# Kernel optimization log

Measured on AMD Instinct MI355X. Metric: run time of the kernel, lower is better.

## Reference

```python
import jax, jax.numpy as jnp
import numpy as np

N_NODES = 100000
N_EDGES = 3200000
N_GRAPHS = 64
IN_FEATS = 128
DIM = 32
N_LAYERS = 4


def setup_inputs() -> dict:
    key = jax.random.key(0)
    ks = jax.random.split(key, 16)
    x = jax.random.normal(ks[0], (N_NODES, IN_FEATS), dtype=jnp.float32)
    src = jax.random.randint(ks[1], (N_EDGES,), 0, N_NODES)
    dst = jax.random.randint(ks[2], (N_EDGES,), 0, N_NODES)
    graph_ids = jnp.sort(jax.random.randint(ks[3], (N_NODES,), 0, N_GRAPHS))
    s = 1.0 / np.sqrt(IN_FEATS)
    s2 = 1.0 / np.sqrt(DIM)
    Wn0 = jax.random.uniform(ks[4], (IN_FEATS, DIM), jnp.float32, -s, s)
    bn0 = jnp.zeros((DIM,), jnp.float32)
    Ws0 = jax.random.uniform(ks[5], (IN_FEATS, DIM), jnp.float32, -s, s)
    Wn = jax.random.uniform(ks[6], (N_LAYERS - 1, DIM, DIM), jnp.float32, -s2, s2)
    bn = jnp.zeros((N_LAYERS - 1, DIM), jnp.float32)
    Ws = jax.random.uniform(ks[7], (N_LAYERS - 1, DIM, DIM), jnp.float32, -s2, s2)
    Wfc1 = jax.random.uniform(ks[8], (DIM, 8), jnp.float32, -s2, s2)
    bfc1 = jnp.zeros((8,), jnp.float32)
    Wout = jax.random.uniform(ks[9], (8, 4), jnp.float32, -1/np.sqrt(8), 1/np.sqrt(8))
    bout = jnp.zeros((4,), jnp.float32)
    return {"x": x, "Wn0": Wn0, "bn0": bn0, "Ws0": Ws0,
            "Wn": Wn, "bn": bn, "Ws": Ws,
            "Wfc1": Wfc1, "bfc1": bfc1, "Wout": Wout, "bout": bout,
            "src": src, "dst": dst, "graph_ids": graph_ids}


def _conv_layer(h, Wn_, bn_, Ws_, src, dst):
    # GraphConv(norm='none'): transform then sum over incoming edges (src -> dst)
    rhs = h @ Wn_                                   # [N, out]
    neigh = jax.ops.segment_sum(rhs[src], dst, num_segments=N_NODES) + bn_
    self_feat = h @ Ws_                             # Linear, no bias
    return jax.nn.relu(neigh + self_feat)


def reference(x, Wn0, bn0, Ws0, Wn, bn, Ws, Wfc1, bfc1, Wout, bout, src, dst, graph_ids):
    h = _conv_layer(x, Wn0, bn0, Ws0, src, dst)
    for i in range(N_LAYERS - 1):
        h = _conv_layer(h, Wn[i], bn[i], Ws[i], src, dst)
    # per-graph sum pooling (dgl.sum_nodes over batched graph)
    hg = jax.ops.segment_sum(h, graph_ids, num_segments=N_GRAPHS)  # [G, 32]
    hg2 = jax.nn.relu(hg @ Wfc1 + bfc1)
    out = jax.nn.relu(hg2 @ Wout + bout)
    return jax.nn.softmax(out, axis=1)
```

## Files before the change

kernel.cpp:

```cpp
#include <hip/hip_runtime.h>
#include <hip/hip_bf16.h>
#include <math.h>


#define TILE_NODES 256
#define CE 12800
#define SCAN_CHUNK 2048
#define MAX_NB 1024
#define SENT 131071

__device__ inline unsigned char f2fp8(float f) {
    unsigned u = __float_as_uint(f);
    unsigned s = (u >> 24) & 0x80u;
    float a = fminf(fabsf(f), 448.f);
    unsigned v = __float_as_uint(a * 0x1p-120f);
    v = v + 0xFFFFFu + ((v >> 20) & 1u);
    return (unsigned char)(s | ((v >> 20) & 0x7Fu));
}
__device__ inline float fp8_dec(unsigned x) {
    unsigned v = ((x & 0x80u) << 24) | ((x & 0x7Fu) << 20);
    return __uint_as_float(v) * 0x1p120f;
}

typedef float v2f __attribute__((ext_vector_type(2)));
typedef _Float16 h2 __attribute__((ext_vector_type(2)));
typedef __fp16 p2 __attribute__((ext_vector_type(2)));
union U32H2 { unsigned u; h2 h; p2 p; };

__device__ inline unsigned packh2(float a, float b) {
#if __has_builtin(__builtin_amdgcn_cvt_pkrtz)
    U32H2 t; t.p = __builtin_amdgcn_cvt_pkrtz(a, b); return t.u;
#else
    U32H2 t; t.h.x = (_Float16)a; t.h.y = (_Float16)b; return t.u;
#endif
}
__device__ inline float dot2(unsigned a, unsigned b, float c) {
    U32H2 ua, ub; ua.u = a; ub.u = b;
#if __has_builtin(__builtin_amdgcn_fdot2)
    return __builtin_amdgcn_fdot2(ua.h, ub.h, c, false);
#else
    return c + (float)ua.h.x * (float)ub.h.x + (float)ua.h.y * (float)ub.h.y;
#endif
}

__device__ inline void acc8_fp8(unsigned w0, unsigned w1, float4& a0, float4& a1) {
#if __has_builtin(__builtin_amdgcn_cvt_pk_f32_fp8)
    v2f p0 = __builtin_amdgcn_cvt_pk_f32_fp8(w0, 0);
    v2f p1 = __builtin_amdgcn_cvt_pk_f32_fp8(w0, 1);
    v2f p2v = __builtin_amdgcn_cvt_pk_f32_fp8(w1, 0);
    v2f p3 = __builtin_amdgcn_cvt_pk_f32_fp8(w1, 1);
    a0.x += p0.x; a0.y += p0.y; a0.z += p1.x; a0.w += p1.y;
    a1.x += p2v.x; a1.y += p2v.y; a1.z += p3.x; a1.w += p3.y;
#else
    a0.x += fp8_dec(w0 & 0xFFu);         a0.y += fp8_dec((w0 >> 8) & 0xFFu);
    a0.z += fp8_dec((w0 >> 16) & 0xFFu); a0.w += fp8_dec(w0 >> 24);
    a1.x += fp8_dec(w1 & 0xFFu);         a1.y += fp8_dec((w1 >> 8) & 0xFFu);
    a1.z += fp8_dec((w1 >> 16) & 0xFFu); a1.w += fp8_dec(w1 >> 24);
#endif
}

__global__ __launch_bounds__(1024) void k_hist2(
    const int* __restrict__ dst, int* __restrict__ histT,
    int n_edges, int NB, int C)
{
    __shared__ int hist[MAX_NB];
    const int c = blockIdx.x;
    for (int b = threadIdx.x; b < NB; b += 1024) hist[b] = 0;
    __syncthreads();
    const int beg = c * CE;
    const int end = min(beg + CE, n_edges);
    for (int e = beg + threadIdx.x; e < end; e += 1024)
        atomicAdd(&hist[dst[e] >> 8], 1);
    __syncthreads();
    for (int b = threadIdx.x; b < NB; b += 1024)
        histT[b * C + c] = hist[b];
}

__global__ __launch_bounds__(256) void k_chunk_sum(
    const int* __restrict__ v, int* __restrict__ part, int n)
{
    __shared__ int red[256];
    const int base = blockIdx.x * SCAN_CHUNK;
    int s = 0;
    for (int i = threadIdx.x; i < SCAN_CHUNK; i += 256) {
        int idx = base + i;
        if (idx < n) s += v[idx];
    }
    red[threadIdx.x] = s;
    __syncthreads();
    for (int off = 128; off > 0; off >>= 1) {
        if (threadIdx.x < off) red[threadIdx.x] += red[threadIdx.x + off];
        __syncthreads();
    }
    if (threadIdx.x == 0) part[blockIdx.x] = red[0];
}

__global__ void k_scan_part(int* __restrict__ part, int nparts)
{
    if (threadIdx.x == 0 && blockIdx.x == 0) {
        int run = 0;
        for (int i = 0; i < nparts; ++i) { int v = part[i]; part[i] = run; run += v; }
    }
}

__global__ __launch_bounds__(256) void k_write_off(
    const int* __restrict__ v, const int* __restrict__ part,
    int* __restrict__ off, int n, int total)
{
    __shared__ int lds[256];
    const int tid   = threadIdx.x;
    const int base  = blockIdx.x * SCAN_CHUNK;
    const int tbase = base + tid * 8;
    int c[8];
    int tot = 0;
#pragma unroll
    for (int m = 0; m < 8; ++m) {
        int idx = tbase + m;
        c[m] = (idx < n) ? v[idx] : 0;
        tot += c[m];
    }
    lds[tid] = tot;
    __syncthreads();
    for (int o = 1; o < 256; o <<= 1) {
        int val = (tid >= o) ? lds[tid - o] : 0;
        __syncthreads();
        lds[tid] += val;
        __syncthreads();
    }
    int run = part[blockIdx.x] + lds[tid] - tot;
#pragma unroll
    for (int m = 0; m < 8; ++m) {
        int idx = tbase + m;
        if (idx < n) off[idx] = run;
        run += c[m];
    }
    if (blockIdx.x == 0 && tid == 0) off[n] = total;
}

__global__ __launch_bounds__(1024) void k_binfill(
    const int* __restrict__ src, const int* __restrict__ dst,
    const int* __restrict__ off, unsigned int* __restrict__ ebuf,
    int n_edges, int NB, int C)
{
    __shared__ int lcur[MAX_NB];
    const int c = blockIdx.x;
    for (int b = threadIdx.x; b < NB; b += 1024)
        lcur[b] = off[b * C + c];
    __syncthreads();
    const int beg = c * CE;
    const int end = min(beg + CE, n_edges);
    for (int e = beg + threadIdx.x; e < end; e += 1024) {
        const int d = dst[e];
        const int b = d >> 8;
        const unsigned int dl = (unsigned int)(d & 255);
        const int pos = atomicAdd(&lcur[b], 1);
        ebuf[pos] = (dl << 17) | (unsigned int)src[e];
    }
}

__global__ __launch_bounds__(1024) void k_tile_sort(
    const int* __restrict__ off, const unsigned int* __restrict__ ebuf,
    int* __restrict__ eidx, int* __restrict__ ptrb, int* __restrict__ ptre,
    int n_nodes, int NB, int C, int n_edges)
{
    __shared__ int hist[TILE_NODES];
    __shared__ int phist[TILE_NODES];
    __shared__ int scan[TILE_NODES];
    __shared__ int cur[TILE_NODES];
    const int t = blockIdx.x;
    const int beg = off[t * C];
    const int end = (t + 1 < NB) ? off[(t + 1) * C] : n_edges;
    const int tb  = ((beg + 3) & ~3) + 1024 * t;
    const int node_base = t * TILE_NODES;
    const int n_valid = min(TILE_NODES, n_nodes - node_base);

    if (threadIdx.x < TILE_NODES) hist[threadIdx.x] = 0;
    __syncthreads();
    for (int e = beg + threadIdx.x; e < end; e += 1024)
        atomicAdd(&hist[ebuf[e] >> 17], 1);
    __syncthreads();
    if (threadIdx.x < TILE_NODES) {
        const int ph = (hist[threadIdx.x] + 3) & ~3;
        phist[threadIdx.x] = ph;
        scan[threadIdx.x]  = ph;
    }
    __syncthreads();
    for (int o = 1; o < TILE_NODES; o <<= 1) {
        int v = 0;
        if (threadIdx.x < TILE_NODES && threadIdx.x >= o) v = scan[threadIdx.x - o];
        __syncthreads();
        if (threadIdx.x < TILE_NODES) scan[threadIdx.x] += v;
        __syncthreads();
    }
    if (threadIdx.x < TILE_NODES) {
        const int ex = scan[threadIdx.x] - phist[threadIdx.x];
        cur[threadIdx.x] = ex;
        if (threadIdx.x < n_valid) {
            ptrb[node_base + threadIdx.x] = tb + ex;
            ptre[node_base + threadIdx.x] = tb + ex + phist[threadIdx.x];
        }
    }
    __syncthreads();
    for (int e = beg + threadIdx.x; e < end; e += 1024) {
        const unsigned int v = ebuf[e];
        const int dl = (int)(v >> 17);
        const int pos = tb + atomicAdd(&cur[dl], 1);
        eidx[pos] = (int)(v & 0x1FFFFu);
    }
    __syncthreads();
    if (threadIdx.x < n_valid) {
        int p  = tb + cur[threadIdx.x];
        const int pe = tb + scan[threadIdx.x];
        for (; p < pe; ++p) eidx[p] = SENT;
    }
}

__global__ __launch_bounds__(256, 4) void k_layer0(
    const float* __restrict__ x, const float* __restrict__ Wn0,
    const float* __restrict__ bn0, const float* __restrict__ Ws0,
    unsigned char* __restrict__ Ab, float* __restrict__ B, int n_nodes)
{
    __shared__ unsigned sWn[64 * 32];
    __shared__ unsigned sWs[64 * 32];
    __shared__ unsigned sx[32 * 64];

    for (int i = threadIdx.x; i < 64 * 32; i += 256) {
        const int k2 = i >> 5, jj = i & 31;
        sWn[i] = packh2(Wn0[(2 * k2) * 32 + jj], Wn0[(2 * k2 + 1) * 32 + jj]);
        sWs[i] = packh2(Ws0[(2 * k2) * 32 + jj], Ws0[(2 * k2 + 1) * 32 + jj]);
    }
    const int tile = blockIdx.x * 32;
    {
        const float4* s4 = (const float4*)(x + (size_t)tile * 128);
        const int lim = (n_nodes - tile) * 32;
#pragma unroll
        for (int m = 0; m < 4; ++m) {
            int i = threadIdx.x + m * 256;
            if (i < lim) {
                float4 v = s4[i];
                const int row = i >> 5, q = i & 31;
                sx[row * 64 + 2 * q]     = packh2(v.x, v.y);
                sx[row * 64 + 2 * q + 1] = packh2(v.z, v.w);
            }
        }
    }
    const int j = threadIdx.x & 31;
    const int r = threadIdx.x >> 5;
    const float bias = bn0[j];
    __syncthreads();

    float accA[4] = {0.f, 0.f, 0.f, 0.f};
    float accB[4] = {bias, bias, bias, bias};
#pragma unroll 2
    for (int k2 = 0; k2 < 64; k2 += 4) {
        const unsigned wn0 = sWn[(k2 + 0) * 32 + j], ws0 = sWs[(k2 + 0) * 32 + j];
        const unsigned wn1 = sWn[(k2 + 1) * 32 + j], ws1 = sWs[(k2 + 1) * 32 + j];
        const unsigned wn2 = sWn[(k2 + 2) * 32 + j], ws2 = sWs[(k2 + 2) * 32 + j];
        const unsigned wn3 = sWn[(k2 + 3) * 32 + j], ws3 = sWs[(k2 + 3) * 32 + j];
#pragma unroll
        for (int m = 0; m < 4; ++m) {
            const uint4 xv = *(const uint4*)(sx + (r + 8 * m) * 64 + k2);
            accA[m] = dot2(xv.x, wn0, accA[m]);
            accA[m] = dot2(xv.y, wn1, accA[m]);
            accA[m] = dot2(xv.z, wn2, accA[m]);
            accA[m] = dot2(xv.w, wn3, accA[m]);
            accB[m] = dot2(xv.x, ws0, accB[m]);
            accB[m] = dot2(xv.y, ws1, accB[m]);
            accB[m] = dot2(xv.z, ws2, accB[m]);
            accB[m] = dot2(xv.w, ws3, accB[m]);
        }
    }
#pragma unroll
    for (int m = 0; m < 4; ++m) {
        const int node = tile + r + 8 * m;
        if (node < n_nodes) {
            Ab[(size_t)node * 32 + j] = f2fp8(accA[m]);
            B[(size_t)node * 32 + j] = accB[m];
        }
    }
}

__global__ __launch_bounds__(256, 4) void k_layer(
    float* HB,
    const float* __restrict__ Wn, const float* __restrict__ bnv,
    const float* __restrict__ Ws, unsigned char* __restrict__ Ab, int n_nodes)
{
    __shared__ unsigned sWn[16 * 32];
    __shared__ unsigned sWs[16 * 32];
    __shared__ unsigned sh[64 * 16];

    for (int i = threadIdx.x; i < 16 * 32; i += 256) {
        const int k2 = i >> 5, jj = i & 31;
        sWn[i] = packh2(Wn[(2 * k2) * 32 + jj], Wn[(2 * k2 + 1) * 32 + jj]);
        sWs[i] = packh2(Ws[(2 * k2) * 32 + jj], Ws[(2 * k2 + 1) * 32 + jj]);
    }
    const int tile = blockIdx.x * 64;
    {
        const float4* s4 = (const float4*)(HB + (size_t)tile * 32);
        const int lim = (n_nodes - tile) * 8;
#pragma unroll
        for (int m = 0; m < 2; ++m) {
            int i = threadIdx.x + m * 256;
            if (i < lim) {
                float4 v = s4[i];
                v.x = fmaxf(v.x, 0.f); v.y = fmaxf(v.y, 0.f);
                v.z = fmaxf(v.z, 0.f); v.w = fmaxf(v.w, 0.f);
                const int row = i >> 3, q = i & 7;
                sh[row * 16 + 2 * q]     = packh2(v.x, v.y);
                sh[row * 16 + 2 * q + 1] = packh2(v.z, v.w);
            }
        }
    }
    const int j = threadIdx.x & 31;
    const int r = threadIdx.x >> 5;
    const float bias = bnv[j];
    __syncthreads();

    float accA[8] = {0.f};
    float accB[8];
#pragma unroll
    for (int m = 0; m < 8; ++m) accB[m] = bias;
#pragma unroll 2
    for (int k2 = 0; k2 < 16; k2 += 4) {
        const unsigned wn0 = sWn[(k2 + 0) * 32 + j], ws0 = sWs[(k2 + 0) * 32 + j];
        const unsigned wn1 = sWn[(k2 + 1) * 32 + j], ws1 = sWs[(k2 + 1) * 32 + j];
        const unsigned wn2 = sWn[(k2 + 2) * 32 + j], ws2 = sWs[(k2 + 2) * 32 + j];
        const unsigned wn3 = sWn[(k2 + 3) * 32 + j], ws3 = sWs[(k2 + 3) * 32 + j];
#pragma unroll
        for (int m = 0; m < 8; ++m) {
            const uint4 hv = *(const uint4*)(sh + (r + 8 * m) * 16 + k2);
            accA[m] = dot2(hv.x, wn0, accA[m]);
            accA[m] = dot2(hv.y, wn1, accA[m]);
            accA[m] = dot2(hv.z, wn2, accA[m]);
            accA[m] = dot2(hv.w, wn3, accA[m]);
            accB[m] = dot2(hv.x, ws0, accB[m]);
            accB[m] = dot2(hv.y, ws1, accB[m]);
            accB[m] = dot2(hv.z, ws2, accB[m]);
            accB[m] = dot2(hv.w, ws3, accB[m]);
        }
    }
#pragma unroll
    for (int m = 0; m < 8; ++m) {
        const int node = tile + r + 8 * m;
        if (node < n_nodes) {
            Ab[(size_t)node * 32 + j] = f2fp8(accA[m]);
            HB[(size_t)node * 32 + j] = accB[m];
        }
    }
}

__global__ __launch_bounds__(256) void k_agg3(
    const int* __restrict__ ptrb, const int* __restrict__ ptre,
    const int* __restrict__ eidx,
    const unsigned char* __restrict__ Ab, float* __restrict__ B, int n_nodes)
{
    const int g    = blockIdx.x * 64 + (threadIdx.x >> 2);
    const int lane = threadIdx.x & 3;
    if (g >= n_nodes) return;
    const int beg = ptrb[g];
    const int end = ptre[g];
    const uint2* __restrict__ A2 = (const uint2*)Ab;
    const int4* __restrict__ E4 = (const int4*)eidx;
    float4* B4 = (float4*)B;

    float4 a0 = B4[(size_t)g * 8 + lane * 2 + 0];
    float4 a1 = B4[(size_t)g * 8 + lane * 2 + 1];
    int e4 = beg >> 2;
    const int n4 = end >> 2;
    for (; e4 + 4 <= n4; e4 += 4) {
        const int4 q0 = E4[e4 + 0];
        const int4 q1 = E4[e4 + 1];
        const int4 q2 = E4[e4 + 2];
        const int4 q3 = E4[e4 + 3];
        uint2 rw;
        rw = A2[(size_t)q0.x * 4 + lane]; acc8_fp8(rw.x, rw.y, a0, a1);
        rw = A2[(size_t)q0.y * 4 + lane]; acc8_fp8(rw.x, rw.y, a0, a1);
        rw = A2[(size_t)q0.z * 4 + lane]; acc8_fp8(rw.x, rw.y, a0, a1);
        rw = A2[(size_t)q0.w * 4 + lane]; acc8_fp8(rw.x, rw.y, a0, a1);
        rw = A2[(size_t)q1.x * 4 + lane]; acc8_fp8(rw.x, rw.y, a0, a1);
        rw = A2[(size_t)q1.y * 4 + lane]; acc8_fp8(rw.x, rw.y, a0, a1);
        rw = A2[(size_t)q1.z * 4 + lane]; acc8_fp8(rw.x, rw.y, a0, a1);
        rw = A2[(size_t)q1.w * 4 + lane]; acc8_fp8(rw.x, rw.y, a0, a1);
        rw = A2[(size_t)q2.x * 4 + lane]; acc8_fp8(rw.x, rw.y, a0, a1);
        rw = A2[(size_t)q2.y * 4 + lane]; acc8_fp8(rw.x, rw.y, a0, a1);
        rw = A2[(size_t)q2.z * 4 + lane]; acc8_fp8(rw.x, rw.y, a0, a1);
        rw = A2[(size_t)q2.w * 4 + lane]; acc8_fp8(rw.x, rw.y, a0, a1);
        rw = A2[(size_t)q3.x * 4 + lane]; acc8_fp8(rw.x, rw.y, a0, a1);
        rw = A2[(size_t)q3.y * 4 + lane]; acc8_fp8(rw.x, rw.y, a0, a1);
        rw = A2[(size_t)q3.z * 4 + lane]; acc8_fp8(rw.x, rw.y, a0, a1);
        rw = A2[(size_t)q3.w * 4 + lane]; acc8_fp8(rw.x, rw.y, a0, a1);
    }
    for (; e4 < n4; ++e4) {
        const int4 q = E4[e4];
        uint2 rw;
        rw = A2[(size_t)q.x * 4 + lane]; acc8_fp8(rw.x, rw.y, a0, a1);
        rw = A2[(size_t)q.y * 4 + lane]; acc8_fp8(rw.x, rw.y, a0, a1);
        rw = A2[(size_t)q.z * 4 + lane]; acc8_fp8(rw.x, rw.y, a0, a1);
        rw = A2[(size_t)q.w * 4 + lane]; acc8_fp8(rw.x, rw.y, a0, a1);
    }
    B4[(size_t)g * 8 + lane * 2 + 0] = a0;
    B4[(size_t)g * 8 + lane * 2 + 1] = a1;
}

__global__ __launch_bounds__(256) void k_zero_f(float* __restrict__ p, int n)
{
    int i = blockIdx.x * 256 + threadIdx.x;
    if (i < n) p[i] = 0.f;
}

__global__ __launch_bounds__(256) void k_pool1(
    const float* __restrict__ H, const int* __restrict__ gids,
    float* __restrict__ hg, int n_nodes)
{
    const int base = blockIdx.x * 128;
    const int lim  = min(base + 128, n_nodes);
    const int j = threadIdx.x & 31;
    const int r = threadIdx.x >> 5;

    int curg = -1;
    float acc = 0.f;
    for (int n = base + r; n < lim; n += 8) {
        const int g = gids[n];
        const float v = fmaxf(H[(size_t)n * 32 + j], 0.f);
        if (g != curg) {
            if (curg >= 0) atomicAdd(&hg[curg * 32 + j], acc);
            curg = g;
            acc = v;
        } else {
            acc += v;
        }
    }
    if (curg >= 0) atomicAdd(&hg[curg * 32 + j], acc);
}

__global__ __launch_bounds__(64) void k_head(
    const float* __restrict__ hg,
    const float* __restrict__ Wfc1, const float* __restrict__ bfc1,
    const float* __restrict__ Wout, const float* __restrict__ bout,
    float* __restrict__ out, int n_graphs)
{
    const int g = blockIdx.x * blockDim.x + threadIdx.x;
    if (g >= n_graphs) return;
    float h[32];
#pragma unroll
    for (int k = 0; k < 32; ++k) h[k] = hg[g * 32 + k];
    float z[8];
#pragma unroll
    for (int m = 0; m < 8; ++m) {
        float a = bfc1[m];
#pragma unroll
        for (int k = 0; k < 32; ++k) a += h[k] * Wfc1[k * 8 + m];
        z[m] = fmaxf(a, 0.f);
    }
    float o[4];
#pragma unroll
    for (int q = 0; q < 4; ++q) {
        float a = bout[q];
#pragma unroll
        for (int m = 0; m < 8; ++m) a += z[m] * Wout[m * 4 + q];
        o[q] = fmaxf(a, 0.f);
    }
    const float mx = fmaxf(fmaxf(o[0], o[1]), fmaxf(o[2], o[3]));
    const float e0 = expf(o[0] - mx), e1 = expf(o[1] - mx);
    const float e2 = expf(o[2] - mx), e3 = expf(o[3] - mx);
    const float inv = 1.f / (e0 + e1 + e2 + e3);
    out[g * 4 + 0] = e0 * inv;
    out[g * 4 + 1] = e1 * inv;
    out[g * 4 + 2] = e2 * inv;
    out[g * 4 + 3] = e3 * inv;
}

extern "C" void kernel_launch(void* const* d_in, const int* in_sizes, int n_in,
                              void* d_out, int out_size, void* d_ws, size_t ws_size,
                              hipStream_t stream)
{
    const float* x    = (const float*)d_in[0];
    const float* Wn0  = (const float*)d_in[1];
    const float* bn0  = (const float*)d_in[2];
    const float* Ws0  = (const float*)d_in[3];
    const float* Wn   = (const float*)d_in[4];
    const float* bn   = (const float*)d_in[5];
    const float* Ws   = (const float*)d_in[6];
    const float* Wfc1 = (const float*)d_in[7];
    const float* bfc1 = (const float*)d_in[8];
    const float* Wout = (const float*)d_in[9];
    const float* bout = (const float*)d_in[10];
    const int*   src  = (const int*)d_in[11];
    const int*   dst  = (const int*)d_in[12];
    const int*   gids = (const int*)d_in[13];

    const int n_nodes  = in_sizes[0] / 128;
    const int n_edges  = in_sizes[11];
    const int n_graphs = out_size / 4;
    const size_t N32 = (size_t)n_nodes * 32;
    const size_t AB_ROWS = 131072;

    const int NB = (n_nodes + TILE_NODES - 1) / TILE_NODES;
    const int C  = (n_edges + CE - 1) / CE;
    const int n_off = NB * C;

    unsigned char* Ab = (unsigned char*)d_ws;
    float* B   = (float*)(Ab + AB_ROWS * 32);
    float* hg  = B + N32;
    int* histT = (int*)(hg + (size_t)n_graphs * 32);
    int* off   = histT + n_off;
    int* part  = off + n_off + 1;
    int* ptrb  = part + 256;
    int* ptre  = ptrb + n_nodes;
    unsigned int* ebuf = (unsigned int*)(ptre + n_nodes);
    int* eidx  = (int*)(ebuf + n_edges);

    const int nparts = (n_off + SCAN_CHUNK - 1) / SCAN_CHUNK;

    k_hist2<<<C, 1024, 0, stream>>>(dst, histT, n_edges, NB, C);
    k_chunk_sum<<<nparts, 256, 0, stream>>>(histT, part, n_off);
    k_scan_part<<<1, 64, 0, stream>>>(part, nparts);
    k_write_off<<<nparts, 256, 0, stream>>>(histT, part, off, n_off, n_edges);
    k_binfill<<<C, 1024, 0, stream>>>(src, dst, off, ebuf, n_edges, NB, C);
    k_tile_sort<<<NB, 1024, 0, stream>>>(off, ebuf, eidx, ptrb, ptre,
                                         n_nodes, NB, C, n_edges);
    k_zero_f<<<1, 256, 0, stream>>>((float*)(Ab + (size_t)SENT * 32), 8);

    const int mblocks0 = (n_nodes + 31) / 32;
    const int mblocks  = (n_nodes + 63) / 64;
    const int ablocks  = (n_nodes + 63) / 64;

    k_layer0<<<mblocks0, 256, 0, stream>>>(x, Wn0, bn0, Ws0, Ab, B, n_nodes);
    k_agg3<<<ablocks, 256, 0, stream>>>(ptrb, ptre, eidx, Ab, B, n_nodes);

    for (int l = 0; l < 3; ++l) {
        k_layer<<<mblocks, 256, 0, stream>>>(B, Wn + l * 1024, bn + l * 32,
                                             Ws + l * 1024, Ab, n_nodes);
        k_agg3<<<ablocks, 256, 0, stream>>>(ptrb, ptre, eidx, Ab, B, n_nodes);
    }

    k_zero_f<<<(n_graphs * 32 + 255) / 256, 256, 0, stream>>>(hg, n_graphs * 32);
    k_pool1<<<(n_nodes + 127) / 128, 256, 0, stream>>>(B, gids, hg, n_nodes);
    k_head<<<(n_graphs + 63) / 64, 64, 0, stream>>>(hg, Wfc1, bfc1, Wout, bout,
                                                    (float*)d_out, n_graphs);
}
```

Before: 367.6 us.

## Use MFMA f16 matrix cores for per-layer node transforms with prepacked weights

Replaces the dot2-based scalar matmuls in the layer kernels with 16x16x32 f16 MFMA instructions, with each wave handling 16 nodes. A new small kernel prepacks the weights once into MFMA B-fragment layout in fp16, so blocks no longer rebuild shared-memory weight tables. Layer 0 now processes 64 nodes per block and uses an XOR-swizzled shared tile to limit bank conflicts. The workspace is also realigned to 256-byte boundaries. The dense transforms are a small share of the total next to the edge aggregation and sorting, so the overall effect is bounded.

Result: faster. 348.5 us (-5.2%).

```diff
diff --git a/kernel.cpp b/kernel.cpp
--- a/kernel.cpp
+++ b/kernel.cpp
@@ -25,21 +25,16 @@
 typedef float v2f __attribute__((ext_vector_type(2)));
 typedef _Float16 h2 __attribute__((ext_vector_type(2)));
 typedef __fp16 p2 __attribute__((ext_vector_type(2)));
+typedef _Float16 f16x8 __attribute__((ext_vector_type(8)));
+typedef float f32x4v __attribute__((ext_vector_type(4)));
 union U32H2 { unsigned u; h2 h; p2 p; };
+union UF { uint4 u; f16x8 h; };
 
 __device__ inline unsigned packh2(float a, float b) {
 #if __has_builtin(__builtin_amdgcn_cvt_pkrtz)
     U32H2 t; t.p = __builtin_amdgcn_cvt_pkrtz(a, b); return t.u;
 #else
     U32H2 t; t.h.x = (_Float16)a; t.h.y = (_Float16)b; return t.u;
-#endif
-}
-__device__ inline float dot2(unsigned a, unsigned b, float c) {
-    U32H2 ua, ub; ua.u = a; ub.u = b;
-#if __has_builtin(__builtin_amdgcn_fdot2)
-    return __builtin_amdgcn_fdot2(ua.h, ub.h, c, false);
-#else
-    return c + (float)ua.h.x * (float)ub.h.x + (float)ua.h.y * (float)ub.h.y;
 #endif
 }
 
@@ -215,85 +210,106 @@
     }
 }
 
+__global__ __launch_bounds__(64) void k_wprep(
+    const float* __restrict__ Wn0, const float* __restrict__ Ws0,
+    const float* __restrict__ Wn, const float* __restrict__ Ws,
+    unsigned char* __restrict__ wf0, unsigned char* __restrict__ wfl)
+{
+    const int f = blockIdx.x;
+    const int l = threadIdx.x;
+    const int n15 = l & 15, quad = l >> 4;
+    unsigned u[4];
+    if (f < 16) {
+        const int mat = f >> 3, t = (f >> 2) & 1, c = f & 3;
+        const float* W = mat ? Ws0 : Wn0;
+        const int n = 16 * t + n15;
+#pragma unroll
+        for (int p = 0; p < 4; ++p) {
+            const int k = c * 32 + quad * 8 + 2 * p;
+            u[p] = packh2(W[k * 32 + n], W[(k + 1) * 32 + n]);
+        }
+        *(uint4*)(wf0 + f * 1024 + l * 16) = make_uint4(u[0], u[1], u[2], u[3]);
+    } else {
+        const int g = f - 16;
+        const int L = g >> 2, ff = g & 3;
+        const int mat = ff >> 1, t = ff & 1;
+        const float* W = (mat ? Ws : Wn) + L * 1024;
+        const int n = 16 * t + n15;
+#pragma unroll
+        for (int p = 0; p < 4; ++p) {
+            const int k = quad * 8 + 2 * p;
+            u[p] = packh2(W[k * 32 + n], W[(k + 1) * 32 + n]);
+        }
+        *(uint4*)(wfl + (size_t)g * 1024 + l * 16) = make_uint4(u[0], u[1], u[2], u[3]);
+    }
+}
+
 __global__ __launch_bounds__(256, 4) void k_layer0(
-    const float* __restrict__ x, const float* __restrict__ Wn0,
-    const float* __restrict__ bn0, const float* __restrict__ Ws0,
+    const float* __restrict__ x, const unsigned char* __restrict__ wf0,
+    const float* __restrict__ bn0,
     unsigned char* __restrict__ Ab, float* __restrict__ B, int n_nodes)
 {
-    __shared__ unsigned sWn[64 * 32];
-    __shared__ unsigned sWs[64 * 32];
-    __shared__ unsigned sx[32 * 64];
-
-    for (int i = threadIdx.x; i < 64 * 32; i += 256) {
-        const int k2 = i >> 5, jj = i & 31;
-        sWn[i] = packh2(Wn0[(2 * k2) * 32 + jj], Wn0[(2 * k2 + 1) * 32 + jj]);
-        sWs[i] = packh2(Ws0[(2 * k2) * 32 + jj], Ws0[(2 * k2 + 1) * 32 + jj]);
-    }
-    const int tile = blockIdx.x * 32;
+    __shared__ unsigned char sxh[64 * 256];
+    const int tile = blockIdx.x * 64;
     {
         const float4* s4 = (const float4*)(x + (size_t)tile * 128);
         const int lim = (n_nodes - tile) * 32;
 #pragma unroll
-        for (int m = 0; m < 4; ++m) {
+        for (int m = 0; m < 8; ++m) {
             int i = threadIdx.x + m * 256;
             if (i < lim) {
                 float4 v = s4[i];
-                const int row = i >> 5, q = i & 31;
-                sx[row * 64 + 2 * q]     = packh2(v.x, v.y);
-                sx[row * 64 + 2 * q + 1] = packh2(v.z, v.w);
+                const int row = i >> 5, kq = i & 31;
+                const int c = kq >> 3;
+                unsigned* wp = (unsigned*)(sxh + row * 256 +
+                                           ((c ^ (row & 1)) * 64) + (kq & 7) * 8);
+                wp[0] = packh2(v.x, v.y);
+                wp[1] = packh2(v.z, v.w);
             }
         }
     }
-    const int j = threadIdx.x & 31;
-    const int r = threadIdx.x >> 5;
-    const float bias = bn0[j];
-    __syncthreads();
-
-    float accA[4] = {0.f, 0.f, 0.f, 0.f};
-    float accB[4] = {bias, bias, bias, bias};
-#pragma unroll 2
-    for (int k2 = 0; k2 < 64; k2 += 4) {
-        const unsigned wn0 = sWn[(k2 + 0) * 32 + j], ws0 = sWs[(k2 + 0) * 32 + j];
-        const unsigned wn1 = sWn[(k2 + 1) * 32 + j], ws1 = sWs[(k2 + 1) * 32 + j];
-        const unsigned wn2 = sWn[(k2 + 2) * 32 + j], ws2 = sWs[(k2 + 2) * 32 + j];
-        const unsigned wn3 = sWn[(k2 + 3) * 32 + j], ws3 = sWs[(k2 + 3) * 32 + j];
-#pragma unroll
-        for (int m = 0; m < 4; ++m) {
-            const uint4 xv = *(const uint4*)(sx + (r + 8 * m) * 64 + k2);
-            accA[m] = dot2(xv.x, wn0, accA[m]);
-            accA[m] = dot2(xv.y, wn1, accA[m]);
-            accA[m] = dot2(xv.z, wn2, accA[m]);
-            accA[m] = dot2(xv.w, wn3, accA[m]);
-            accB[m] = dot2(xv.x, ws0, accB[m]);
-            accB[m] = dot2(xv.y, ws1, accB[m]);
-            accB[m] = dot2(xv.z, ws2, accB[m]);
-            accB[m] = dot2(xv.w, ws3, accB[m]);
-        }
-    }
-#pragma unroll
-    for (int m = 0; m < 4; ++m) {
-        const int node = tile + r + 8 * m;
+    const int l = threadIdx.x & 63;
+    const int w = threadIdx.x >> 6;
+    const int n15 = l & 15, quad = l >> 4;
+    UF bf[16];
+#pragma unroll
+    for (int f = 0; f < 16; ++f)
+        bf[f].u = *(const uint4*)(wf0 + f * 1024 + l * 16);
+    const float bias0 = bn0[n15];
+    const float bias1 = bn0[16 + n15];
+    __syncthreads();
+
+    f32x4v aN0 = {0.f, 0.f, 0.f, 0.f}, aN1 = {0.f, 0.f, 0.f, 0.f};
+    f32x4v aS0 = {bias0, bias0, bias0, bias0};
+    f32x4v aS1 = {bias1, bias1, bias1, bias1};
+    const int row = w * 16 + n15;
+#pragma unroll
+    for (int c = 0; c < 4; ++c) {
+        UF a;
+        a.u = *(const uint4*)(sxh + row * 256 + ((c ^ (row & 1)) * 64) + quad * 16);
+        aN0 = __builtin_amdgcn_mfma_f32_16x16x32_f16(a.h, bf[c].h,      aN0, 0, 0, 0);
+        aN1 = __builtin_amdgcn_mfma_f32_16x16x32_f16(a.h, bf[4 + c].h,  aN1, 0, 0, 0);
+        aS0 = __builtin_amdgcn_mfma_f32_16x16x32_f16(a.h, bf[8 + c].h,  aS0, 0, 0, 0);
+        aS1 = __builtin_amdgcn_mfma_f32_16x16x32_f16(a.h, bf[12 + c].h, aS1, 0, 0, 0);
+    }
+#pragma unroll
+    for (int r = 0; r < 4; ++r) {
+        const int node = tile + w * 16 + quad * 4 + r;
         if (node < n_nodes) {
-            Ab[(size_t)node * 32 + j] = f2fp8(accA[m]);
-            B[(size_t)node * 32 + j] = accB[m];
+            B[(size_t)node * 32 + n15]      = aS0[r];
+            B[(size_t)node * 32 + 16 + n15] = aS1[r];
+            Ab[(size_t)node * 32 + n15]      = f2fp8(aN0[r]);
+            Ab[(size_t)node * 32 + 16 + n15] = f2fp8(aN1[r]);
         }
     }
 }
 
 __global__ __launch_bounds__(256, 4) void k_layer(
-    float* HB,
-    const float* __restrict__ Wn, const float* __restrict__ bnv,
-    const float* __restrict__ Ws, unsigned char* __restrict__ Ab, int n_nodes)
-{
-    __shared__ unsigned sWn[16 * 32];
-    __shared__ unsigned sWs[16 * 32];
-    __shared__ unsigned sh[64 * 16];
-
-    for (int i = threadIdx.x; i < 16 * 32; i += 256) {
-        const int k2 = i >> 5, jj = i & 31;
-        sWn[i] = packh2(Wn[(2 * k2) * 32 + jj], Wn[(2 * k2 + 1) * 32 + jj]);
-        sWs[i] = packh2(Ws[(2 * k2) * 32 + jj], Ws[(2 * k2 + 1) * 32 + jj]);
-    }
+    float* HB, const unsigned char* __restrict__ wfl,
+    const float* __restrict__ bnv,
+    unsigned char* __restrict__ Ab, int n_nodes)
+{
+    __shared__ unsigned char shh[64 * 64];
     const int tile = blockIdx.x * 64;
     {
         const float4* s4 = (const float4*)(HB + (size_t)tile * 32);
@@ -306,45 +322,42 @@
                 v.x = fmaxf(v.x, 0.f); v.y = fmaxf(v.y, 0.f);
                 v.z = fmaxf(v.z, 0.f); v.w = fmaxf(v.w, 0.f);
                 const int row = i >> 3, q = i & 7;
-                sh[row * 16 + 2 * q]     = packh2(v.x, v.y);
-                sh[row * 16 + 2 * q + 1] = packh2(v.z, v.w);
+                unsigned* wp = (unsigned*)(shh + row * 64 + q * 8);
+                wp[0] = packh2(v.x, v.y);
+                wp[1] = packh2(v.z, v.w);
             }
         }
     }
-    const int j = threadIdx.x & 31;
-    const int r = threadIdx.x >> 5;
-    const float bias = bnv[j];
-    __syncthreads();
-
-    float accA[8] = {0.f};
-    float accB[8];
-#pragma unroll
-    for (int m = 0; m < 8; ++m) accB[m] = bias;
-#pragma unroll 2
-    for (int k2 = 0; k2 < 16; k2 += 4) {
-        const unsigned wn0 = sWn[(k2 + 0) * 32 + j], ws0 = sWs[(k2 + 0) * 32 + j];
-        const unsigned wn1 = sWn[(k2 + 1) * 32 + j], ws1 = sWs[(k2 + 1) * 32 + j];
-        const unsigned wn2 = sWn[(k2 + 2) * 32 + j], ws2 = sWs[(k2 + 2) * 32 + j];
-        const unsigned wn3 = sWn[(k2 + 3) * 32 + j], ws3 = sWs[(k2 + 3) * 32 + j];
-#pragma unroll
-        for (int m = 0; m < 8; ++m) {
-            const uint4 hv = *(const uint4*)(sh + (r + 8 * m) * 16 + k2);
-            accA[m] = dot2(hv.x, wn0, accA[m]);
-            accA[m] = dot2(hv.y, wn1, accA[m]);
-            accA[m] = dot2(hv.z, wn2, accA[m]);
-            accA[m] = dot2(hv.w, wn3, accA[m]);
-            accB[m] = dot2(hv.x, ws0, accB[m]);
-            accB[m] = dot2(hv.y, ws1, accB[m]);
-            accB[m] = dot2(hv.z, ws2, accB[m]);
-            accB[m] = dot2(hv.w, ws3, accB[m]);
-        }
-    }
-#pragma unroll
-    for (int m = 0; m < 8; ++m) {
-        const int node = tile + r + 8 * m;
+    const int l = threadIdx.x & 63;
+    const int w = threadIdx.x >> 6;
+    const int n15 = l & 15, quad = l >> 4;
+    UF b0, b1, b2, b3;
+    b0.u = *(const uint4*)(wfl + 0 * 1024 + l * 16);
+    b1.u = *(const uint4*)(wfl + 1 * 1024 + l * 16);
+    b2.u = *(const uint4*)(wfl + 2 * 1024 + l * 16);
+    b3.u = *(const uint4*)(wfl + 3 * 1024 + l * 16);
+    const float bias0 = bnv[n15];
+    const float bias1 = bnv[16 + n15];
+    __syncthreads();
+
+    const int row = w * 16 + n15;
+    UF a;
+    a.u = *(const uint4*)(shh + row * 64 + quad * 16);
+    f32x4v aN0 = {0.f, 0.f, 0.f, 0.f}, aN1 = {0.f, 0.f, 0.f, 0.f};
+    f32x4v aS0 = {bias0, bias0, bias0, bias0};
+    f32x4v aS1 = {bias1, bias1, bias1, bias1};
+    aN0 = __builtin_amdgcn_mfma_f32_16x16x32_f16(a.h, b0.h, aN0, 0, 0, 0);
+    aN1 = __builtin_amdgcn_mfma_f32_16x16x32_f16(a.h, b1.h, aN1, 0, 0, 0);
+    aS0 = __builtin_amdgcn_mfma_f32_16x16x32_f16(a.h, b2.h, aS0, 0, 0, 0);
+    aS1 = __builtin_amdgcn_mfma_f32_16x16x32_f16(a.h, b3.h, aS1, 0, 0, 0);
+#pragma unroll
+    for (int r = 0; r < 4; ++r) {
+        const int node = tile + w * 16 + quad * 4 + r;
         if (node < n_nodes) {
-            Ab[(size_t)node * 32 + j] = f2fp8(accA[m]);
-            HB[(size_t)node * 32 + j] = accB[m];
+            HB[(size_t)node * 32 + n15]      = aS0[r];
+            HB[(size_t)node * 32 + 16 + n15] = aS1[r];
+            Ab[(size_t)node * 32 + n15]      = f2fp8(aN0[r]);
+            Ab[(size_t)node * 32 + 16 + n15] = f2fp8(aN1[r]);
         }
     }
 }
@@ -499,16 +512,22 @@
     const int C  = (n_edges + CE - 1) / CE;
     const int n_off = NB * C;
 
-    unsigned char* Ab = (unsigned char*)d_ws;
-    float* B   = (float*)(Ab + AB_ROWS * 32);
-    float* hg  = B + N32;
-    int* histT = (int*)(hg + (size_t)n_graphs * 32);
-    int* off   = histT + n_off;
-    int* part  = off + n_off + 1;
-    int* ptrb  = part + 256;
-    int* ptre  = ptrb + n_nodes;
-    unsigned int* ebuf = (unsigned int*)(ptre + n_nodes);
-    int* eidx  = (int*)(ebuf + n_edges);
+    char* p = (char*)d_ws;
+    auto alloc = [&](size_t bytes) {
+        char* r = p; p += (bytes + 255) & ~(size_t)255; return r;
+    };
+    unsigned char* Ab  = (unsigned char*)alloc(AB_ROWS * 32);
+    float* B           = (float*)alloc(N32 * 4);
+    float* hg          = (float*)alloc((size_t)n_graphs * 32 * 4);
+    int* histT         = (int*)alloc((size_t)n_off * 4);
+    int* off           = (int*)alloc(((size_t)n_off + 1) * 4);
+    int* part          = (int*)alloc(256 * 4);
+    int* ptrb          = (int*)alloc((size_t)n_nodes * 4);
+    int* ptre          = (int*)alloc((size_t)n_nodes * 4);
+    unsigned char* wf0 = (unsigned char*)alloc(16 * 1024);
+    unsigned char* wfl = (unsigned char*)alloc(12 * 1024);
+    unsigned int* ebuf = (unsigned int*)alloc((size_t)n_edges * 4);
+    int* eidx          = (int*)alloc(((size_t)n_edges + 1024 * (size_t)NB + 4) * 4);
 
     const int nparts = (n_off + SCAN_CHUNK - 1) / SCAN_CHUNK;
 
@@ -519,18 +538,18 @@
     k_binfill<<<C, 1024, 0, stream>>>(src, dst, off, ebuf, n_edges, NB, C);
     k_tile_sort<<<NB, 1024, 0, stream>>>(off, ebuf, eidx, ptrb, ptre,
                                          n_nodes, NB, C, n_edges);
+    k_wprep<<<28, 64, 0, stream>>>(Wn0, Ws0, Wn, Ws, wf0, wfl);
     k_zero_f<<<1, 256, 0, stream>>>((float*)(Ab + (size_t)SENT * 32), 8);
 
-    const int mblocks0 = (n_nodes + 31) / 32;
-    const int mblocks  = (n_nodes + 63) / 64;
-    const int ablocks  = (n_nodes + 63) / 64;
-
-    k_layer0<<<mblocks0, 256, 0, stream>>>(x, Wn0, bn0, Ws0, Ab, B, n_nodes);
+    const int mblocks = (n_nodes + 63) / 64;
+    const int ablocks = (n_nodes + 63) / 64;
+
+    k_layer0<<<mblocks, 256, 0, stream>>>(x, wf0, bn0, Ab, B, n_nodes);
     k_agg3<<<ablocks, 256, 0, stream>>>(ptrb, ptre, eidx, Ab, B, n_nodes);
 
     for (int l = 0; l < 3; ++l) {
-        k_layer<<<mblocks, 256, 0, stream>>>(B, Wn + l * 1024, bn + l * 32,
-                                             Ws + l * 1024, Ab, n_nodes);
+        k_layer<<<mblocks, 256, 0, stream>>>(B, wfl + (size_t)l * 4096,
+                                             bn + l * 32, Ab, n_nodes);
         k_agg3<<<ablocks, 256, 0, stream>>>(ptrb, ptre, eidx, Ab, B, n_nodes);
     }
 
```
